# Kernel optimization log

Measured on AMD Instinct MI355X. Metric: run time of the kernel, lower is better.

The kernel has to match this reference:

```python
import jax, jax.numpy as jnp
import numpy as np

T, N, F_IND, F_MAC = 250, 4000, 46, 178
H = 64
F_IN = F_IND + F_MAC  # dense-net input = firm chars + tiled macro = 224


def setup_inputs() -> dict:
    key = jax.random.key(0)
    ks = jax.random.split(key, 9)
    macro_features = jax.random.normal(ks[0], (1, T, F_MAC), jnp.float32)
    individual_features = jax.random.normal(ks[1], (1, T, N, F_IND), jnp.float32)
    masks = jnp.ones((1, T, N, 1), dtype=bool)
    returns_tensor = jax.random.normal(ks[2], (1, T, N, 1), jnp.float32) * 0.05
    W1 = jax.random.normal(ks[3], (F_IN, H), jnp.float32) / np.sqrt(F_IN).astype(np.float32)
    b1 = jnp.zeros((H,), jnp.float32)
    W2 = jax.random.normal(ks[4], (H, H), jnp.float32) / np.sqrt(H).astype(np.float32)
    b2 = jnp.zeros((H,), jnp.float32)
    W3 = jax.random.normal(ks[5], (H, 1), jnp.float32) / np.sqrt(H).astype(np.float32)
    b3 = jnp.zeros((1,), jnp.float32)
    return {"macro_features": macro_features, "individual_features": individual_features,
            "masks": masks, "returns_tensor": returns_tensor,
            "W1": W1, "b1": b1, "W2": W2, "b2": b2, "W3": W3, "b3": b3}


def reference(macro_features, individual_features, masks, returns_tensor, W1, b1, W2, b2, W3, b3):
    B, Tt, Nn, _ = individual_features.shape
    # tile macro state over assets and concat with firm characteristics -> [1,T,N,F_IN]
    mac = jnp.broadcast_to(macro_features[:, :, None, :], (B, Tt, Nn, macro_features.shape[-1]))
    dense_inputs = jnp.concatenate([individual_features, mac], axis=-1)
    mf = masks.astype(dense_inputs.dtype)  # [1,T,N,1]
    # dense net: 2 relu hidden layers + linear head, output_size=1 (SDF weight per firm-month)
    h = jax.nn.relu(dense_inputs @ W1 + b1)
    h = jax.nn.relu(h @ W2 + b2)
    weights = (h @ W3 + b3) * mf  # zero out masked entries (mask is all-ones -> static shape)
    # weighted returns and per-time segment sum (== torch.split + per-segment torch.sum)
    weighted_returns = returns_tensor * weights * mf
    num_val_per_time = jnp.sum(mf[0, :, :, 0], axis=1)  # [T]
    sum_per_time = jnp.sum(weighted_returns[0, :, :, 0], axis=1)  # [T]
    # normalize_w = True
    sum_per_time = sum_per_time / num_val_per_time * jnp.mean(num_val_per_time)
    sdf = (sum_per_time + 1.0)[:, None]  # [T,1]
    weights_flat = weights.reshape(1, Tt * Nn, 1)  # matches masked_select layout (all-true mask)
    return sdf, weights_flat
```

## Files before the change

### kernel.cpp

```cpp
#include <hip/hip_runtime.h>

#define T_DIM 250
#define N_DIM 4000
#define F_IND 46
#define F_MAC 178
#define H_DIM 64

typedef __bf16         bf16x8  __attribute__((ext_vector_type(8)));
typedef float          f32x4   __attribute__((ext_vector_type(4)));
typedef unsigned short ushort8 __attribute__((ext_vector_type(8)));
typedef float          f32x4a8 __attribute__((ext_vector_type(4), aligned(8)));

union FragU { ushort8 u; bf16x8 b; unsigned w[4]; };
union BF2   { unsigned u; __bf16 h[2]; };

__device__ __forceinline__ unsigned short f2bf(float f) {
    unsigned u = __float_as_uint(f);
    return (unsigned short)((u + 0x7fffu + ((u >> 16) & 1u)) >> 16);
}
__device__ __forceinline__ unsigned packbf2(float lo, float hi) {
    BF2 p; p.h[0] = (__bf16)lo; p.h[1] = (__bf16)hi; return p.u;
}

__global__ __launch_bounds__(256)
void prep_kernel(const float* __restrict__ mac,
                 const float* __restrict__ W1,
                 const float* __restrict__ b1,
                 const float* __restrict__ W2,
                 unsigned short* __restrict__ Wb1,
                 unsigned short* __restrict__ Wb2,
                 float* __restrict__ Mproj,
                 float* __restrict__ sdf)
{
    const int b = blockIdx.x;
    const int tid = threadIdx.x;
    if (b < 2) {
        const float* W = (b == 0) ? W1 : W2;
        unsigned short* dst = (b == 0) ? Wb1 : Wb2;
        const int kmax = (b == 0) ? F_IND : H_DIM;
        for (int idx = tid; idx < 4096; idx += 256) {
            int j  = idx & 7;
            int L  = (idx >> 3) & 63;
            int rt = (idx >> 9) & 3;
            int s  = idx >> 11;
            int k  = s * 32 + ((L >> 4) * 8) + j;
            int c  = rt * 16 + (L & 15);
            float v = (k < kmax) ? W[k * H_DIM + c] : 0.0f;
            dst[idx] = f2bf(v);
        }
    } else {
        __shared__ float red[4][H_DIM];
        const int t  = b - 2;
        const int j  = tid & 63;
        const int kc = tid >> 6;
        const int k0 = kc * 45;
        const int k1 = (k0 + 45 < F_MAC) ? k0 + 45 : F_MAC;
        float acc = (kc == 0) ? b1[j] : 0.0f;
        const float* mrow = mac + t * F_MAC;
        for (int k = k0; k < k1; ++k)
            acc = fmaf(mrow[k], W1[(F_IND + k) * H_DIM + j], acc);
        red[kc][j] = acc;
        __syncthreads();
        if (tid < 64) {
            Mproj[t * H_DIM + j] = red[0][j] + red[1][j] + red[2][j] + red[3][j];
            if (tid == 0) sdf[t] = 1.0f;
        }
    }
}

__global__ __launch_bounds__(256, 4)
void mlp_mfma(const float* __restrict__ ind,
              const float* __restrict__ ret,
              const unsigned short* __restrict__ Wb1,
              const unsigned short* __restrict__ Wb2,
              const float* __restrict__ Mproj,
              const float* __restrict__ b2,
              const float* __restrict__ W3,
              const float* __restrict__ b3,
              float* __restrict__ out_w,
              float* __restrict__ sdf)
{
    __shared__ unsigned Hsh[128 * 32];

    const int tid  = threadIdx.x;
    const int lane = tid & 63;
    const int w    = tid >> 6;
    const int q    = lane >> 4;
    const int m    = lane & 15;
    const int m7   = m & 7;
    const int t    = blockIdx.y;
    const int nwv  = blockIdx.x * 128 + w * 32;

    if (nwv >= N_DIM) return;
    const int rbase = w * 32;

    const float retv = (lane < 32) ? ret[(size_t)t * N_DIM + nwv + lane] : 0.0f;

    const float* xr = ind + ((size_t)t * N_DIM + (nwv + m)) * F_IND;
    const int CTS = 16 * F_IND;

    f32x4a8 xa[2], xb[2];
    #pragma unroll
    for (int ct = 0; ct < 2; ++ct) {
        const float* p = xr + ct * CTS + q * 8;
        xa[ct] = *(const f32x4a8*)(p);
        xb[ct] = *(const f32x4a8*)(p + 4);
    }
    f32x4a8 ya[2] = {}, yb[2] = {};
    if (q == 0) {
        #pragma unroll
        for (int ct = 0; ct < 2; ++ct) {
            ya[ct] = *(const f32x4a8*)(xr + ct * CTS + 32);
            yb[ct] = *(const f32x4a8*)(xr + ct * CTS + 36);
        }
    } else if (q == 1) {
        #pragma unroll
        for (int ct = 0; ct < 2; ++ct) {
            ya[ct] = *(const f32x4a8*)(xr + ct * CTS + 40);
            float2 z = *(const float2*)(xr + ct * CTS + 44);
            yb[ct][0] = z.x; yb[ct][1] = z.y;
        }
    }

    FragU a1[8];
    #pragma unroll
    for (int f = 0; f < 8; ++f)
        a1[f].u = *(const ushort8*)(Wb1 + (f * 64 + lane) * 8);

    f32x4 acc[4][2];
    #pragma unroll
    for (int rt = 0; rt < 4; ++rt) {
        f32x4 mpv = *(const f32x4*)(Mproj + t * H_DIM + rt * 16 + q * 4);
        acc[rt][0] = mpv;
        acc[rt][1] = mpv;
    }

    FragU xf[2], yf[2];
    #pragma unroll
    for (int ct = 0; ct < 2; ++ct)
        #pragma unroll
        for (int i = 0; i < 4; ++i) {
            xf[ct].b[i]     = (__bf16)xa[ct][i];
            xf[ct].b[i + 4] = (__bf16)xb[ct][i];
            yf[ct].b[i]     = (__bf16)ya[ct][i];
            yf[ct].b[i + 4] = (__bf16)yb[ct][i];
        }

    #pragma unroll
    for (int rt = 0; rt < 4; ++rt)
        #pragma unroll
        for (int ct = 0; ct < 2; ++ct)
            acc[rt][ct] = __builtin_amdgcn_mfma_f32_16x16x32_bf16(
                a1[rt].b, xf[ct].b, acc[rt][ct], 0, 0, 0);
    #pragma unroll
    for (int rt = 0; rt < 4; ++rt)
        #pragma unroll
        for (int ct = 0; ct < 2; ++ct)
            acc[rt][ct] = __builtin_amdgcn_mfma_f32_16x16x32_bf16(
                a1[4 + rt].b, yf[ct].b, acc[rt][ct], 0, 0, 0);

    FragU a2[8];
    #pragma unroll
    for (int f = 0; f < 8; ++f)
        a2[f].u = *(const ushort8*)(Wb2 + (f * 64 + lane) * 8);
    f32x4 bb2[4];
    #pragma unroll
    for (int rt = 0; rt < 4; ++rt)
        bb2[rt] = *(const f32x4*)(b2 + rt * 16 + q * 4);

    #pragma unroll
    for (int rt = 0; rt < 4; ++rt)
        #pragma unroll
        for (int ct = 0; ct < 2; ++ct) {
            int sl = ct * 16 + m;
            unsigned lo = packbf2(fmaxf(acc[rt][ct][0], 0.0f),
                                  fmaxf(acc[rt][ct][1], 0.0f));
            unsigned hi = packbf2(fmaxf(acc[rt][ct][2], 0.0f),
                                  fmaxf(acc[rt][ct][3], 0.0f));
            int phys = ((rt * 2 + (q >> 1)) ^ m7) * 4 + (q & 1) * 2;
            uint2 v; v.x = lo; v.y = hi;
            *(uint2*)(Hsh + (rbase + sl) * 32 + phys) = v;
        }

    #pragma unroll
    for (int rt = 0; rt < 4; ++rt)
        #pragma unroll
        for (int ct = 0; ct < 2; ++ct)
            acc[rt][ct] = bb2[rt];

    #pragma unroll
    for (int s = 0; s < 2; ++s) {
        FragU hf[2];
        #pragma unroll
        for (int ct = 0; ct < 2; ++ct) {
            int sl  = ct * 16 + m;
            int blk = (s * 4 + q) ^ m7;
            hf[ct].u = *(const ushort8*)(Hsh + (rbase + sl) * 32 + blk * 4);
        }
        #pragma unroll
        for (int rt = 0; rt < 4; ++rt)
            #pragma unroll
            for (int ct = 0; ct < 2; ++ct)
                acc[rt][ct] = __builtin_amdgcn_mfma_f32_16x16x32_bf16(
                    a2[s * 4 + rt].b, hf[ct].b, acc[rt][ct], 0, 0, 0);
    }

    float wv;
    {
        f32x4 w3[4];
        #pragma unroll
        for (int rt = 0; rt < 4; ++rt)
            w3[rt] = *(const f32x4*)(W3 + rt * 16 + q * 4);
        const float b3s = b3[0];

        float pq[2];
        #pragma unroll
        for (int ct = 0; ct < 2; ++ct) {
            float p = 0.0f;
            #pragma unroll
            for (int rt = 0; rt < 4; ++rt)
                #pragma unroll
                for (int r = 0; r < 4; ++r)
                    p = fmaf(fmaxf(acc[rt][ct][r], 0.0f), w3[rt][r], p);
            p += __shfl_xor(p, 16, 64);
            p += __shfl_xor(p, 32, 64);
            pq[ct] = p;
        }
        wv = ((q & 1) ? pq[1] : pq[0]) + b3s;
    }

    float contrib = 0.0f;
    if (lane < 32) {
        out_w[(size_t)t * N_DIM + nwv + lane] = wv;
        contrib = retv * wv;
    }
    #pragma unroll
    for (int off = 16; off > 0; off >>= 1)
        contrib += __shfl_down(contrib, off, 64);
    if (lane == 0) atomicAdd(&sdf[t], contrib);
}

extern "C" void kernel_launch(void* const* d_in, const int* in_sizes, int n_in,
                              void* d_out, int out_size, void* d_ws, size_t ws_size,
                              hipStream_t stream) {
    (void)in_sizes; (void)n_in; (void)out_size; (void)ws_size;

    const float* mac = (const float*)d_in[0];
    const float* ind = (const float*)d_in[1];
    const float* ret = (const float*)d_in[3];
    const float* W1  = (const float*)d_in[4];
    const float* b1  = (const float*)d_in[5];
    const float* W2  = (const float*)d_in[6];
    const float* b2  = (const float*)d_in[7];
    const float* W3  = (const float*)d_in[8];
    const float* b3  = (const float*)d_in[9];

    float* sdf   = (float*)d_out;
    float* out_w = (float*)d_out + T_DIM;

    unsigned short* Wb1 = (unsigned short*)d_ws;
    unsigned short* Wb2 = Wb1 + 4096;
    float* Mproj = (float*)((char*)d_ws + 16384);

    prep_kernel<<<dim3(252), 256, 0, stream>>>(mac, W1, b1, W2, Wb1, Wb2, Mproj, sdf);

    dim3 grid(32, T_DIM);
    mlp_mfma<<<grid, 256, 0, stream>>>(ind, ret, Wb1, Wb2, Mproj, b2, W3, b3,
                                       out_w, sdf);
}
```

Before: 361.2 us.

## Stage input rows via global_load_lds and process 64 assets per wave

Each wave now copies its contiguous 64-row slab of firm characteristics directly into LDS with the buffer-to-LDS load instruction, instead of issuing strided per-lane vector loads from global memory. It then builds the bf16 MFMA fragments from LDS. Each wave also covers 64 assets instead of 32, which halves the grid and amortizes the weight-fragment loads over more work. The cost is more LDS and more registers per wave, so the occupancy hint drops from 4 to 3 blocks. The loads clamp their offsets for the partial tail slab.

```diff
diff --git a/kernel.cpp b/kernel.cpp
--- a/kernel.cpp
+++ b/kernel.cpp
@@ -9,7 +9,6 @@
 typedef __bf16         bf16x8  __attribute__((ext_vector_type(8)));
 typedef float          f32x4   __attribute__((ext_vector_type(4)));
 typedef unsigned short ushort8 __attribute__((ext_vector_type(8)));
-typedef float          f32x4a8 __attribute__((ext_vector_type(4), aligned(8)));
 
 union FragU { ushort8 u; bf16x8 b; unsigned w[4]; };
 union BF2   { unsigned u; __bf16 h[2]; };
@@ -68,7 +67,7 @@
     }
 }
 
-__global__ __launch_bounds__(256, 4)
+__global__ __launch_bounds__(256, 3)
 void mlp_mfma(const float* __restrict__ ind,
               const float* __restrict__ ret,
               const unsigned short* __restrict__ Wb1,
@@ -80,7 +79,7 @@
               float* __restrict__ out_w,
               float* __restrict__ sdf)
 {
-    __shared__ unsigned Hsh[128 * 32];
+    __shared__ unsigned Lds[4 * 2944];
 
     const int tid  = threadIdx.x;
     const int lane = tid & 63;
@@ -89,36 +88,29 @@
     const int m    = lane & 15;
     const int m7   = m & 7;
     const int t    = blockIdx.y;
-    const int nwv  = blockIdx.x * 128 + w * 32;
+    const int nwv  = blockIdx.x * 256 + w * 64;
 
     if (nwv >= N_DIM) return;
-    const int rbase = w * 32;
-
-    const float retv = (lane < 32) ? ret[(size_t)t * N_DIM + nwv + lane] : 0.0f;
-
-    const float* xr = ind + ((size_t)t * N_DIM + (nwv + m)) * F_IND;
-    const int CTS = 16 * F_IND;
-
-    f32x4a8 xa[2], xb[2];
-    #pragma unroll
-    for (int ct = 0; ct < 2; ++ct) {
-        const float* p = xr + ct * CTS + q * 8;
-        xa[ct] = *(const f32x4a8*)(p);
-        xb[ct] = *(const f32x4a8*)(p + 4);
-    }
-    f32x4a8 ya[2] = {}, yb[2] = {};
-    if (q == 0) {
-        #pragma unroll
-        for (int ct = 0; ct < 2; ++ct) {
-            ya[ct] = *(const f32x4a8*)(xr + ct * CTS + 32);
-            yb[ct] = *(const f32x4a8*)(xr + ct * CTS + 36);
-        }
-    } else if (q == 1) {
-        #pragma unroll
-        for (int ct = 0; ct < 2; ++ct) {
-            ya[ct] = *(const f32x4a8*)(xr + ct * CTS + 40);
-            float2 z = *(const float2*)(xr + ct * CTS + 44);
-            yb[ct][0] = z.x; yb[ct][1] = z.y;
+
+    unsigned* WB = Lds + w * 2944;
+    const int valid = (N_DIM - nwv < 64) ? (N_DIM - nwv) : 64;
+    const int limB  = valid * 184;
+
+    {
+        const char* src = (const char*)ind + ((size_t)t * N_DIM + nwv) * (F_IND * 4);
+        #pragma unroll
+        for (int i = 0; i < 11; ++i) {
+            int o = i * 1024 + lane * 16;
+            if (o > limB - 16) o = limB - 16;
+            __builtin_amdgcn_global_load_lds((const unsigned*)(src + o),
+                                             WB + i * 256, 16, 0, 0);
+        }
+        #pragma unroll
+        for (int i = 0; i < 2; ++i) {
+            int o = 11264 + i * 256 + lane * 4;
+            if (o > limB - 4) o = limB - 4;
+            __builtin_amdgcn_global_load_lds((const unsigned*)(src + o),
+                                             WB + 2816 + i * 64, 4, 0, 0);
         }
     }
 
@@ -126,36 +118,65 @@
     #pragma unroll
     for (int f = 0; f < 8; ++f)
         a1[f].u = *(const ushort8*)(Wb1 + (f * 64 + lane) * 8);
-
-    f32x4 acc[4][2];
-    #pragma unroll
-    for (int rt = 0; rt < 4; ++rt) {
-        f32x4 mpv = *(const f32x4*)(Mproj + t * H_DIM + rt * 16 + q * 4);
-        acc[rt][0] = mpv;
-        acc[rt][1] = mpv;
-    }
-
-    FragU xf[2], yf[2];
-    #pragma unroll
-    for (int ct = 0; ct < 2; ++ct)
-        #pragma unroll
-        for (int i = 0; i < 4; ++i) {
-            xf[ct].b[i]     = (__bf16)xa[ct][i];
-            xf[ct].b[i + 4] = (__bf16)xb[ct][i];
-            yf[ct].b[i]     = (__bf16)ya[ct][i];
-            yf[ct].b[i + 4] = (__bf16)yb[ct][i];
-        }
-
-    #pragma unroll
-    for (int rt = 0; rt < 4; ++rt)
-        #pragma unroll
-        for (int ct = 0; ct < 2; ++ct)
+    f32x4 mp[4];
+    #pragma unroll
+    for (int rt = 0; rt < 4; ++rt)
+        mp[rt] = *(const f32x4*)(Mproj + t * H_DIM + rt * 16 + q * 4);
+    const int nlane = nwv + lane;
+    const float retv = (nlane < N_DIM) ? ret[(size_t)t * N_DIM + nlane] : 0.0f;
+
+    asm volatile("s_waitcnt vmcnt(0)" ::: "memory");
+    __builtin_amdgcn_sched_barrier(0);
+
+    FragU xf[4], yf[4] = {};
+    #pragma unroll
+    for (int ct = 0; ct < 4; ++ct) {
+        const unsigned* rowp = WB + (ct * 16 + m) * 46;
+        const float2* p = (const float2*)(rowp + q * 8);
+        float2 v0 = p[0], v1 = p[1], v2 = p[2], v3 = p[3];
+        xf[ct].b[0] = (__bf16)v0.x; xf[ct].b[1] = (__bf16)v0.y;
+        xf[ct].b[2] = (__bf16)v1.x; xf[ct].b[3] = (__bf16)v1.y;
+        xf[ct].b[4] = (__bf16)v2.x; xf[ct].b[5] = (__bf16)v2.y;
+        xf[ct].b[6] = (__bf16)v3.x; xf[ct].b[7] = (__bf16)v3.y;
+    }
+    if (q == 0) {
+        #pragma unroll
+        for (int ct = 0; ct < 4; ++ct) {
+            const float2* p = (const float2*)(WB + (ct * 16 + m) * 46 + 32);
+            float2 v0 = p[0], v1 = p[1], v2 = p[2], v3 = p[3];
+            yf[ct].b[0] = (__bf16)v0.x; yf[ct].b[1] = (__bf16)v0.y;
+            yf[ct].b[2] = (__bf16)v1.x; yf[ct].b[3] = (__bf16)v1.y;
+            yf[ct].b[4] = (__bf16)v2.x; yf[ct].b[5] = (__bf16)v2.y;
+            yf[ct].b[6] = (__bf16)v3.x; yf[ct].b[7] = (__bf16)v3.y;
+        }
+    } else if (q == 1) {
+        #pragma unroll
+        for (int ct = 0; ct < 4; ++ct) {
+            const float2* p = (const float2*)(WB + (ct * 16 + m) * 46 + 40);
+            float2 v0 = p[0], v1 = p[1], v2 = p[2];
+            yf[ct].b[0] = (__bf16)v0.x; yf[ct].b[1] = (__bf16)v0.y;
+            yf[ct].b[2] = (__bf16)v1.x; yf[ct].b[3] = (__bf16)v1.y;
+            yf[ct].b[4] = (__bf16)v2.x; yf[ct].b[5] = (__bf16)v2.y;
+        }
+    }
+
+    f32x4 acc[4][4];
+    #pragma unroll
+    for (int rt = 0; rt < 4; ++rt)
+        #pragma unroll
+        for (int ct = 0; ct < 4; ++ct)
+            acc[rt][ct] = mp[rt];
+
+    #pragma unroll
+    for (int rt = 0; rt < 4; ++rt)
+        #pragma unroll
+        for (int ct = 0; ct < 4; ++ct)
             acc[rt][ct] = __builtin_amdgcn_mfma_f32_16x16x32_bf16(
                 a1[rt].b, xf[ct].b, acc[rt][ct], 0, 0, 0);
     #pragma unroll
     for (int rt = 0; rt < 4; ++rt)
         #pragma unroll
-        for (int ct = 0; ct < 2; ++ct)
+        for (int ct = 0; ct < 4; ++ct)
             acc[rt][ct] = __builtin_amdgcn_mfma_f32_16x16x32_bf16(
                 a1[4 + rt].b, yf[ct].b, acc[rt][ct], 0, 0, 0);
 
@@ -171,7 +192,7 @@
     #pragma unroll
     for (int rt = 0; rt < 4; ++rt)
         #pragma unroll
-        for (int ct = 0; ct < 2; ++ct) {
+        for (int ct = 0; ct < 4; ++ct) {
             int sl = ct * 16 + m;
             unsigned lo = packbf2(fmaxf(acc[rt][ct][0], 0.0f),
                                   fmaxf(acc[rt][ct][1], 0.0f));
@@ -179,28 +200,28 @@
                                   fmaxf(acc[rt][ct][3], 0.0f));
             int phys = ((rt * 2 + (q >> 1)) ^ m7) * 4 + (q & 1) * 2;
             uint2 v; v.x = lo; v.y = hi;
-            *(uint2*)(Hsh + (rbase + sl) * 32 + phys) = v;
-        }
-
-    #pragma unroll
-    for (int rt = 0; rt < 4; ++rt)
-        #pragma unroll
-        for (int ct = 0; ct < 2; ++ct)
+            *(uint2*)(WB + sl * 32 + phys) = v;
+        }
+
+    #pragma unroll
+    for (int rt = 0; rt < 4; ++rt)
+        #pragma unroll
+        for (int ct = 0; ct < 4; ++ct)
             acc[rt][ct] = bb2[rt];
 
     #pragma unroll
     for (int s = 0; s < 2; ++s) {
-        FragU hf[2];
-        #pragma unroll
-        for (int ct = 0; ct < 2; ++ct) {
+        FragU hf[4];
+        #pragma unroll
+        for (int ct = 0; ct < 4; ++ct) {
             int sl  = ct * 16 + m;
             int blk = (s * 4 + q) ^ m7;
-            hf[ct].u = *(const ushort8*)(Hsh + (rbase + sl) * 32 + blk * 4);
+            hf[ct].u = *(const ushort8*)(WB + sl * 32 + blk * 4);
         }
         #pragma unroll
         for (int rt = 0; rt < 4; ++rt)
             #pragma unroll
-            for (int ct = 0; ct < 2; ++ct)
+            for (int ct = 0; ct < 4; ++ct)
                 acc[rt][ct] = __builtin_amdgcn_mfma_f32_16x16x32_bf16(
                     a2[s * 4 + rt].b, hf[ct].b, acc[rt][ct], 0, 0, 0);
     }
@@ -213,9 +234,9 @@
             w3[rt] = *(const f32x4*)(W3 + rt * 16 + q * 4);
         const float b3s = b3[0];
 
-        float pq[2];
-        #pragma unroll
-        for (int ct = 0; ct < 2; ++ct) {
+        float pq[4];
+        #pragma unroll
+        for (int ct = 0; ct < 4; ++ct) {
             float p = 0.0f;
             #pragma unroll
             for (int rt = 0; rt < 4; ++rt)
@@ -226,16 +247,17 @@
             p += __shfl_xor(p, 32, 64);
             pq[ct] = p;
         }
-        wv = ((q & 1) ? pq[1] : pq[0]) + b3s;
+        wv = (q == 0) ? pq[0] : (q == 1) ? pq[1] : (q == 2) ? pq[2] : pq[3];
+        wv += b3s;
     }
 
     float contrib = 0.0f;
-    if (lane < 32) {
-        out_w[(size_t)t * N_DIM + nwv + lane] = wv;
+    if (nlane < N_DIM) {
+        out_w[(size_t)t * N_DIM + nlane] = wv;
         contrib = retv * wv;
     }
     #pragma unroll
-    for (int off = 16; off > 0; off >>= 1)
+    for (int off = 32; off > 0; off >>= 1)
         contrib += __shfl_down(contrib, off, 64);
     if (lane == 0) atomicAdd(&sdf[t], contrib);
 }
@@ -264,7 +286,7 @@
 
     prep_kernel<<<dim3(252), 256, 0, stream>>>(mac, W1, b1, W2, Wb1, Wb2, Mproj, sdf);
 
-    dim3 grid(32, T_DIM);
+    dim3 grid((N_DIM + 255) / 256, T_DIM);
     mlp_mfma<<<grid, 256, 0, stream>>>(ind, ret, Wb1, Wb2, Mproj, b2, W3, b3,
                                        out_w, sdf);
 }
```

After: 317.1 us. 12.2% less time.
